# Optimization experiments

Measured on AMD Instinct MI355X. Metric: run time of the kernel, lower is better.

Reference implementation:

```python
import jax, jax.numpy as jnp
import numpy as np

HEADS = 4


def setup_inputs() -> dict:
    key = jax.random.key(0)
    ks = jax.random.split(key, 5)
    B, T, C, H, W = 2, 16, 256, 64, 64
    x = jax.random.normal(ks[0], (B, T, C, H, W), dtype=jnp.float32)
    s = 1.0 / np.sqrt(C).astype(np.float32)  # kaiming-ish init scale for 1x1 conv
    Wq = jax.random.normal(ks[1], (C, C), dtype=jnp.float32) * s
    Wk = jax.random.normal(ks[2], (C, C), dtype=jnp.float32) * s
    Wv = jax.random.normal(ks[3], (C, C), dtype=jnp.float32) * s
    Wp = jax.random.normal(ks[4], (C, C), dtype=jnp.float32) * s
    return {"x": x, "Wq": Wq, "Wk": Wk, "Wv": Wv, "Wp": Wp}


def reference(x, Wq, Wk, Wv, Wp):
    B, T, C, H, W = x.shape
    heads = HEADS
    Ch = C // heads
    scale = Ch ** (-0.5)
    # [B,T,C,H,W] -> [B*H*W, T, C]: each spatial pixel has a T x C temporal track
    xf = jnp.transpose(x, (0, 3, 4, 1, 2)).reshape(B * H * W, T, C)
    # Conv1d(C,C,1,bias=False) == channel matmul: out[n,t,d] = sum_c W[d,c] x[n,t,c]
    q = jnp.einsum('ntc,dc->ntd', xf, Wq).reshape(-1, T, heads, Ch) * scale
    k = jnp.einsum('ntc,dc->ntd', xf, Wk).reshape(-1, T, heads, Ch)
    v = jnp.einsum('ntc,dc->ntd', xf, Wv).reshape(-1, T, heads, Ch)
    k_soft = jax.nn.softmax(k, axis=1)    # softmax over time T (torch dim=-1 of [n,h,c,t])
    q_soft = jax.nn.softmax(q, axis=-1)   # softmax over head channels Ch (torch dim=-2)
    # linear attention: outer-product context then query contraction
    kv = jnp.einsum('nthc,nthd->nhcd', k_soft, v)         # [N,h,Ch,Ch]
    out = jnp.einsum('nthc,nhcd->nthd', q_soft, kv)       # [N,T,h,Ch]
    out = out.reshape(-1, T, C)
    out = jnp.einsum('ntc,dc->ntd', out, Wp)
    out = out.reshape(B, H, W, T, C)
    return jnp.transpose(out, (0, 3, 4, 1, 2))
```

## Files before the change

### kernel.cpp

```cpp
#include <hip/hip_runtime.h>
#include <hip/hip_bf16.h>

#define DI __device__ __forceinline__

typedef __attribute__((ext_vector_type(8))) short bf16x8;
typedef __attribute__((ext_vector_type(4))) float f32x4;
typedef __attribute__((ext_vector_type(4))) _Float16 f16x4;

constexpr int XPAD = 264;
constexpr float LOG2E = 1.4426950408889634f;

DI short f2bf(float f) {
  __hip_bfloat16 h = __float2bfloat16(f);
  union { __hip_bfloat16 h; short s; } c; c.h = h; return c.s;
}

DI unsigned pk2(float a, float b) {
  union { __hip_bfloat162 h; unsigned u; } c;
  c.h.x = __float2bfloat16(a); c.h.y = __float2bfloat16(b);
  return c.u;
}

DI short f2h(float f) {
  _Float16 h = (_Float16)f;
  union { _Float16 h; short s; } c; c.h = h; return c.s;
}

DI f16x4 pkh4(float a, float b, float c, float d) {
  auto lo = __builtin_amdgcn_cvt_pkrtz(a, b);
  auto hi = __builtin_amdgcn_cvt_pkrtz(c, d);
  union { struct { decltype(lo) l, h; } p; f16x4 v; } u;
  u.p.l = lo; u.p.h = hi;
  return u.v;
}

DI f16x4 ld4h(const short* p) {
  union { uint2 u; f16x4 v; } c;
  c.u = *(const uint2*)p;
  return c.v;
}

DI f32x4 mfma16(bf16x8 a, bf16x8 b, f32x4 c) {
  return __builtin_amdgcn_mfma_f32_16x16x32_bf16(a, b, c, 0, 0, 0);
}

DI f32x4 mfmah(f16x4 a, f16x4 b, f32x4 c) {
  return __builtin_amdgcn_mfma_f32_16x16x16f16(a, b, c, 0, 0, 0);
}

DI f32x4 fzero() { return f32x4{0.f, 0.f, 0.f, 0.f}; }

DI int xsw(int row, int e) { return row * 256 + (e ^ ((row & 7) << 3)); }

__global__ void wconv_kernel(const float* __restrict__ a, const float* __restrict__ b,
                             const float* __restrict__ c, const float* __restrict__ d,
                             short* __restrict__ o) {
  int i = blockIdx.x * 256 + threadIdx.x;
  int mat = i >> 14;
  int off = (i & 16383) * 4;
  const float* s = (mat == 0) ? a : (mat == 1) ? b : (mat == 2) ? c : d;
  const float sc = (mat == 0) ? 0.125f : 1.0f;
  float4 v = *(const float4*)(s + off);
  uint2 r; r.x = pk2(v.x * sc, v.y * sc); r.y = pk2(v.z * sc, v.w * sc);
  *(uint2*)(o + mat * 65536 + off) = r;
}

__global__ __launch_bounds__(256, 2)
void xt_kernel(const float* __restrict__ x, short* __restrict__ xt, int n0chunk) {
  __shared__ short T[64 * 258];
  const int tid = threadIdx.x;
  const int gi  = blockIdx.x >> 4;
  const int t   = blockIdx.x & 15;
  const int n0g = n0chunk + gi * 64;
  const int b   = n0g >> 12;
  const int hw0 = n0g & 4095;
  const float* xb = x + ((size_t)(b * 16 + t) * 256) * 4096 + hw0;

  #pragma unroll
  for (int ci = 0; ci < 16; ++ci) {
    const int c   = ci * 16 + (tid >> 4);
    const int px4 = tid & 15;
    float4 v = *(const float4*)(xb + (size_t)c * 4096 + px4 * 4);
    T[(px4 * 4 + 0) * 258 + c] = f2bf(v.x);
    T[(px4 * 4 + 1) * 258 + c] = f2bf(v.y);
    T[(px4 * 4 + 2) * 258 + c] = f2bf(v.z);
    T[(px4 * 4 + 3) * 258 + c] = f2bf(v.w);
  }
  __syncthreads();

  const int wave = tid >> 6, lane = tid & 63;
  #pragma unroll
  for (int itp = 0; itp < 16; ++itp) {
    const int px  = itp * 4 + wave;
    const int row = (px & 3) * 16 + t;
    const int sw8 = (row & 7) << 3;
    const size_t obase = ((size_t)(gi * 16 + (px >> 2))) * 16384 + row * 256;
    const int dstc = (((lane >> 1) * 8) ^ sw8) + (lane & 1) * 4;
    const int tb = px * 258 + lane * 4;
    union { short s[4]; uint2 u; } pk;
    pk.s[0] = T[tb + 0]; pk.s[1] = T[tb + 1];
    pk.s[2] = T[tb + 2]; pk.s[3] = T[tb + 3];
    *(uint2*)&xt[obase + dstc] = pk.u;
  }
}

__global__ __launch_bounds__(256, 3)
void k1_kernel(const short* __restrict__ xt, const short* __restrict__ wbf,
               short* __restrict__ att) {
  __shared__ short SMEM[16384 + 4096];
  short* Xs = SMEM;

  const int tid  = threadIdx.x;
  const int wave = tid >> 6;
  const int lane = tid & 63;
  const int g    = lane >> 4;
  const int li   = lane & 15;

  short* qs = SMEM + 16384 + wave * 1024;

  int bid = blockIdx.x;
  const int nb = gridDim.x;
  if ((nb & 7) == 0) { const int q = nb >> 3; bid = (bid & 7) * q + (bid >> 3); }

  {
    const short* src = xt + (size_t)bid * 16384 + wave * 512 + lane * 8;
    #pragma unroll
    for (int it = 0; it < 8; ++it) {
      __builtin_amdgcn_global_load_lds(
          (const __attribute__((address_space(1))) void*)(src + it * 2048),
          (__attribute__((address_space(3))) void*)(SMEM + it * 2048 + wave * 512),
          16, 0, 0);
    }
  }
  __syncthreads();

  const short* wq = wbf;
  const short* wk = wbf + 65536;
  const short* wv = wbf + 131072;
  const size_t wrow = (size_t)(wave * 64) * 256;

  f16x4 akf[4][4];
  {
    f32x4 kacc[4][4];
    #pragma unroll
    for (int p = 0; p < 4; ++p)
      #pragma unroll
      for (int nt = 0; nt < 4; ++nt) kacc[p][nt] = fzero();

    __builtin_amdgcn_s_setprio(1);
    #pragma unroll
    for (int ks = 0; ks < 8; ++ks) {
      bf16x8 kb[4];
      #pragma unroll
      for (int nt = 0; nt < 4; ++nt)
        kb[nt] = *(const bf16x8*)(wk + wrow + (size_t)(nt * 16 + li) * 256 + ks * 32 + g * 8);
      #pragma unroll
      for (int p = 0; p < 4; ++p) {
        bf16x8 af = *(const bf16x8*)&Xs[xsw(p * 16 + li, ks * 32 + g * 8)];
        #pragma unroll
        for (int nt = 0; nt < 4; ++nt)
          kacc[p][nt] = mfma16(af, kb[nt], kacc[p][nt]);
      }
    }
    __builtin_amdgcn_s_setprio(0);

    #pragma unroll
    for (int p = 0; p < 4; ++p)
      #pragma unroll
      for (int nt = 0; nt < 4; ++nt) {
        float e0 = exp2f(kacc[p][nt][0] * LOG2E);
        float e1 = exp2f(kacc[p][nt][1] * LOG2E);
        float e2 = exp2f(kacc[p][nt][2] * LOG2E);
        float e3 = exp2f(kacc[p][nt][3] * LOG2E);
        float s = e0 + e1 + e2 + e3;
        s += __shfl_xor(s, 16);
        s += __shfl_xor(s, 32);
        const float inv = 1.f / s;
        akf[p][nt] = pkh4(e0 * inv, e1 * inv, e2 * inv, e3 * inv);
      }
  }

  f16x4 bvf[4][4];
  #pragma unroll
  for (int h = 0; h < 2; ++h) {
    f32x4 vacc[4][2];
    #pragma unroll
    for (int p = 0; p < 4; ++p)
      #pragma unroll
      for (int n2 = 0; n2 < 2; ++n2) vacc[p][n2] = fzero();

    __builtin_amdgcn_s_setprio(1);
    #pragma unroll
    for (int ks = 0; ks < 8; ++ks) {
      bf16x8 vb[2];
      #pragma unroll
      for (int n2 = 0; n2 < 2; ++n2)
        vb[n2] = *(const bf16x8*)(wv + wrow + (size_t)((h * 2 + n2) * 16 + li) * 256 + ks * 32 + g * 8);
      #pragma unroll
      for (int p = 0; p < 4; ++p) {
        bf16x8 af = *(const bf16x8*)&Xs[xsw(p * 16 + li, ks * 32 + g * 8)];
        #pragma unroll
        for (int n2 = 0; n2 < 2; ++n2)
          vacc[p][n2] = mfma16(af, vb[n2], vacc[p][n2]);
      }
    }
    __builtin_amdgcn_s_setprio(0);

    #pragma unroll
    for (int p = 0; p < 4; ++p)
      #pragma unroll
      for (int n2 = 0; n2 < 2; ++n2)
        bvf[p][h * 2 + n2] = pkh4(vacc[p][n2][0], vacc[p][n2][1],
                                  vacc[p][n2][2], vacc[p][n2][3]);
  }

  f32x4 qacc[4][4];
  #pragma unroll
  for (int p = 0; p < 4; ++p)
    #pragma unroll
    for (int nt = 0; nt < 4; ++nt) qacc[p][nt] = fzero();

  __builtin_amdgcn_s_setprio(1);
  #pragma unroll
  for (int ks = 0; ks < 8; ++ks) {
    bf16x8 qb[4];
    #pragma unroll
    for (int nt = 0; nt < 4; ++nt)
      qb[nt] = *(const bf16x8*)(wq + wrow + (size_t)(nt * 16 + li) * 256 + ks * 32 + g * 8);
    #pragma unroll
    for (int p = 0; p < 4; ++p) {
      bf16x8 af = *(const bf16x8*)&Xs[xsw(p * 16 + li, ks * 32 + g * 8)];
      #pragma unroll
      for (int nt = 0; nt < 4; ++nt)
        qacc[p][nt] = mfma16(af, qb[nt], qacc[p][nt]);
    }
  }
  __builtin_amdgcn_s_setprio(0);

  #pragma unroll
  for (int p = 0; p < 4; ++p) {
    #pragma unroll
    for (int r = 0; r < 4; ++r) {
      float e0 = exp2f(qacc[p][0][r] * LOG2E);
      float e1 = exp2f(qacc[p][1][r] * LOG2E);
      float e2 = exp2f(qacc[p][2][r] * LOG2E);
      float e3 = exp2f(qacc[p][3][r] * LOG2E);
      float s = e0 + e1 + e2 + e3;
      s += __shfl_xor(s, 1); s += __shfl_xor(s, 2);
      s += __shfl_xor(s, 4); s += __shfl_xor(s, 8);
      const float inv = 1.f / s;
      const int t = g * 4 + r;
      const int xw = (t & 7) << 3;
      short* dq = qs + t * 64;
      dq[( 0 + li) ^ xw] = f2h(e0 * inv);
      dq[(16 + li) ^ xw] = f2h(e1 * inv);
      dq[(32 + li) ^ xw] = f2h(e2 * inv);
      dq[(48 + li) ^ xw] = f2h(e3 * inv);
    }

    f32x4 oacc[4];
    #pragma unroll
    for (int nt = 0; nt < 4; ++nt) oacc[nt] = fzero();

    #pragma unroll
    for (int cq = 0; cq < 4; ++cq) {
      f32x4 kva[4];
      #pragma unroll
      for (int nt = 0; nt < 4; ++nt)
        kva[nt] = mfmah(akf[p][cq], bvf[p][nt], fzero());
      f16x4 aq = ld4h(qs + li * 64 + (((cq * 16 + g * 4) ^ ((li & 7) << 3))));
      #pragma unroll
      for (int nt = 0; nt < 4; ++nt) {
        f16x4 kb16 = pkh4(kva[nt][0], kva[nt][1], kva[nt][2], kva[nt][3]);
        oacc[nt] = mfmah(aq, kb16, oacc[nt]);
      }
    }

    const size_t arow = ((size_t)bid * 4 + p) * 16;
    #pragma unroll
    for (int nt = 0; nt < 4; ++nt)
      #pragma unroll
      for (int r = 0; r < 4; ++r)
        att[(arow + g * 4 + r) * 256 + wave * 64 + nt * 16 + li] = f2bf(oacc[nt][r]);
  }
}

__global__ __launch_bounds__(256, 2)
void k2_kernel(const short* __restrict__ att, const short* __restrict__ wpb,
               float* __restrict__ out, int n0chunk) {
  __shared__ short A[128 * XPAD];
  const int tid = threadIdx.x;
  const int wave = tid >> 6, lane = tid & 63, g = lane >> 4, li = lane & 15;
  const int pb = blockIdx.x >> 1;
  const int t0 = (blockIdx.x & 1) * 8;
  const int n0 = n0chunk + pb * 16;
  const int b = n0 >> 12, hw0 = n0 & 4095;

  for (int idx = tid; idx < 128 * 32; idx += 256) {
    const int row = idx >> 5, seg = idx & 31;
    const int p = row & 15, tl = row >> 4;
    const short* src = att + ((size_t)((pb * 16 + p) * 16 + t0 + tl)) * 256 + seg * 8;
    *(int4*)&A[row * XPAD + seg * 8] = *(const int4*)src;
  }
  __syncthreads();

  f32x4 acc[8][4];
  #pragma unroll
  for (int mt = 0; mt < 8; ++mt)
    #pragma unroll
    for (int n4 = 0; n4 < 4; ++n4) acc[mt][n4] = fzero();

  #pragma unroll
  for (int ks = 0; ks < 8; ++ks) {
    bf16x8 bf[4];
    #pragma unroll
    for (int n4 = 0; n4 < 4; ++n4)
      bf[n4] = *(const bf16x8*)(wpb + (size_t)((wave * 4 + n4) * 16 + li) * 256 + ks * 32 + g * 8);
    #pragma unroll
    for (int mt = 0; mt < 8; ++mt) {
      bf16x8 af = *(const bf16x8*)&A[(mt * 16 + li) * XPAD + ks * 32 + g * 8];
      #pragma unroll
      for (int n4 = 0; n4 < 4; ++n4) acc[mt][n4] = mfma16(af, bf[n4], acc[mt][n4]);
    }
  }

  float* ob = out + (size_t)b * (16 * 256 * 4096) + hw0;
  #pragma unroll
  for (int mt = 0; mt < 8; ++mt)
    #pragma unroll
    for (int n4 = 0; n4 < 4; ++n4) {
      const int t = t0 + mt;
      const int c = (wave * 4 + n4) * 16 + li;
      float4 v;
      v.x = acc[mt][n4][0]; v.y = acc[mt][n4][1];
      v.z = acc[mt][n4][2]; v.w = acc[mt][n4][3];
      *(float4*)(ob + (size_t)(t * 256 + c) * 4096 + g * 4) = v;
    }
}

extern "C" void kernel_launch(void* const* d_in, const int* in_sizes, int n_in,
                              void* d_out, int out_size, void* d_ws, size_t ws_size,
                              hipStream_t stream) {
  const float* x  = (const float*)d_in[0];
  const float* Wq = (const float*)d_in[1];
  const float* Wk = (const float*)d_in[2];
  const float* Wv = (const float*)d_in[3];
  const float* Wp = (const float*)d_in[4];
  float* out = (float*)d_out;

  short* wbf = (short*)d_ws;
  short* att = wbf + 4 * 65536;

  wconv_kernel<<<256, 256, 0, stream>>>(Wq, Wk, Wv, Wp, wbf);

  const size_t wsAvail = (ws_size > 524288) ? (ws_size - 524288) : 0;
  const size_t perPix = 16 * 256 * 2;
  int chunk = 64;
  while (chunk < 8192 && (size_t)(chunk * 2) * perPix <= wsAvail) chunk <<= 1;

  short* xt = att + (size_t)chunk * 4096;

  for (int n0 = 0; n0 < 8192; n0 += chunk) {
    xt_kernel<<<(chunk / 64) * 16, 256, 0, stream>>>(x, xt, n0);
    k1_kernel<<<chunk / 4, 256, 0, stream>>>(xt, wbf, att);
    k2_kernel<<<(chunk / 16) * 2, 256, 0, stream>>>(att, wbf + 3 * 65536, out, n0);
  }
}
```

Before: 245.9 us.

## Compute q softmax first into global scratch, drop LDS q buffer for occupancy

Moves the Q projection and its channel softmax to the start of k1. The softmaxed q is written to a per-wave global scratch buffer instead of an LDS staging area, and k1 reads it back after a vmcnt wait. This frees LDS and register pressure so launch bounds can rise to 4 blocks per CU. It also replaces exp2f and division with the hardware exp2 and rcp intrinsics. In exchange it adds a global write and read round trip per pixel. It also needs more workspace, which may shrink the chunk size and add kernel launches. Cross-lane visibility through global memory is relied on within a wave.

```diff
diff --git a/kernel.cpp b/kernel.cpp
--- a/kernel.cpp
+++ b/kernel.cpp
@@ -9,6 +9,9 @@
 
 constexpr int XPAD = 264;
 constexpr float LOG2E = 1.4426950408889634f;
+
+DI float fexp(float x) { return __builtin_amdgcn_exp2f(x * LOG2E); }
+DI float frcp(float x) { return __builtin_amdgcn_rcpf(x); }
 
 DI short f2bf(float f) {
   __hip_bfloat16 h = __float2bfloat16(f);
@@ -104,10 +107,10 @@
   }
 }
 
-__global__ __launch_bounds__(256, 3)
+__global__ __launch_bounds__(256, 4)
 void k1_kernel(const short* __restrict__ xt, const short* __restrict__ wbf,
-               short* __restrict__ att) {
-  __shared__ short SMEM[16384 + 4096];
+               short* __restrict__ att, short* __restrict__ qsg) {
+  __shared__ short SMEM[16384];
   short* Xs = SMEM;
 
   const int tid  = threadIdx.x;
@@ -116,8 +119,6 @@
   const int g    = lane >> 4;
   const int li   = lane & 15;
 
-  short* qs = SMEM + 16384 + wave * 1024;
-
   int bid = blockIdx.x;
   const int nb = gridDim.x;
   if ((nb & 7) == 0) { const int q = nb >> 3; bid = (bid & 7) * q + (bid >> 3); }
@@ -138,6 +139,54 @@
   const short* wk = wbf + 65536;
   const short* wv = wbf + 131072;
   const size_t wrow = (size_t)(wave * 64) * 256;
+  short* qsw = qsg + ((size_t)bid * 4 * 4 + wave) * 1024;
+
+  {
+    f32x4 qacc[4][4];
+    #pragma unroll
+    for (int p = 0; p < 4; ++p)
+      #pragma unroll
+      for (int nt = 0; nt < 4; ++nt) qacc[p][nt] = fzero();
+
+    __builtin_amdgcn_s_setprio(1);
+    #pragma unroll
+    for (int ks = 0; ks < 8; ++ks) {
+      bf16x8 qb[4];
+      #pragma unroll
+      for (int nt = 0; nt < 4; ++nt)
+        qb[nt] = *(const bf16x8*)(wq + wrow + (size_t)(nt * 16 + li) * 256 + ks * 32 + g * 8);
+      #pragma unroll
+      for (int p = 0; p < 4; ++p) {
+        bf16x8 af = *(const bf16x8*)&Xs[xsw(p * 16 + li, ks * 32 + g * 8)];
+        #pragma unroll
+        for (int nt = 0; nt < 4; ++nt)
+          qacc[p][nt] = mfma16(af, qb[nt], qacc[p][nt]);
+      }
+    }
+    __builtin_amdgcn_s_setprio(0);
+
+    #pragma unroll
+    for (int p = 0; p < 4; ++p) {
+      short* qsp = qsw + p * 4096;
+      #pragma unroll
+      for (int r = 0; r < 4; ++r) {
+        float e0 = fexp(qacc[p][0][r]);
+        float e1 = fexp(qacc[p][1][r]);
+        float e2 = fexp(qacc[p][2][r]);
+        float e3 = fexp(qacc[p][3][r]);
+        float s = e0 + e1 + e2 + e3;
+        s += __shfl_xor(s, 1); s += __shfl_xor(s, 2);
+        s += __shfl_xor(s, 4); s += __shfl_xor(s, 8);
+        const float inv = frcp(s);
+        const int t = g * 4 + r;
+        short* dst = qsp + t * 64 + li;
+        dst[0]  = f2h(e0 * inv);
+        dst[16] = f2h(e1 * inv);
+        dst[32] = f2h(e2 * inv);
+        dst[48] = f2h(e3 * inv);
+      }
+    }
+  }
 
   f16x4 akf[4][4];
   {
@@ -168,14 +217,14 @@
     for (int p = 0; p < 4; ++p)
       #pragma unroll
       for (int nt = 0; nt < 4; ++nt) {
-        float e0 = exp2f(kacc[p][nt][0] * LOG2E);
-        float e1 = exp2f(kacc[p][nt][1] * LOG2E);
-        float e2 = exp2f(kacc[p][nt][2] * LOG2E);
-        float e3 = exp2f(kacc[p][nt][3] * LOG2E);
+        float e0 = fexp(kacc[p][nt][0]);
+        float e1 = fexp(kacc[p][nt][1]);
+        float e2 = fexp(kacc[p][nt][2]);
+        float e3 = fexp(kacc[p][nt][3]);
         float s = e0 + e1 + e2 + e3;
         s += __shfl_xor(s, 16);
         s += __shfl_xor(s, 32);
-        const float inv = 1.f / s;
+        const float inv = frcp(s);
         akf[p][nt] = pkh4(e0 * inv, e1 * inv, e2 * inv, e3 * inv);
       }
   }
@@ -214,50 +263,11 @@
                                   vacc[p][n2][2], vacc[p][n2][3]);
   }
 
-  f32x4 qacc[4][4];
-  #pragma unroll
-  for (int p = 0; p < 4; ++p)
-    #pragma unroll
-    for (int nt = 0; nt < 4; ++nt) qacc[p][nt] = fzero();
-
-  __builtin_amdgcn_s_setprio(1);
-  #pragma unroll
-  for (int ks = 0; ks < 8; ++ks) {
-    bf16x8 qb[4];
-    #pragma unroll
-    for (int nt = 0; nt < 4; ++nt)
-      qb[nt] = *(const bf16x8*)(wq + wrow + (size_t)(nt * 16 + li) * 256 + ks * 32 + g * 8);
-    #pragma unroll
-    for (int p = 0; p < 4; ++p) {
-      bf16x8 af = *(const bf16x8*)&Xs[xsw(p * 16 + li, ks * 32 + g * 8)];
-      #pragma unroll
-      for (int nt = 0; nt < 4; ++nt)
-        qacc[p][nt] = mfma16(af, qb[nt], qacc[p][nt]);
-    }
-  }
-  __builtin_amdgcn_s_setprio(0);
+  asm volatile("s_waitcnt vmcnt(0)" ::: "memory");
 
   #pragma unroll
   for (int p = 0; p < 4; ++p) {
-    #pragma unroll
-    for (int r = 0; r < 4; ++r) {
-      float e0 = exp2f(qacc[p][0][r] * LOG2E);
-      float e1 = exp2f(qacc[p][1][r] * LOG2E);
-      float e2 = exp2f(qacc[p][2][r] * LOG2E);
-      float e3 = exp2f(qacc[p][3][r] * LOG2E);
-      float s = e0 + e1 + e2 + e3;
-      s += __shfl_xor(s, 1); s += __shfl_xor(s, 2);
-      s += __shfl_xor(s, 4); s += __shfl_xor(s, 8);
-      const float inv = 1.f / s;
-      const int t = g * 4 + r;
-      const int xw = (t & 7) << 3;
-      short* dq = qs + t * 64;
-      dq[( 0 + li) ^ xw] = f2h(e0 * inv);
-      dq[(16 + li) ^ xw] = f2h(e1 * inv);
-      dq[(32 + li) ^ xw] = f2h(e2 * inv);
-      dq[(48 + li) ^ xw] = f2h(e3 * inv);
-    }
-
+    const short* qsp = qsw + p * 4096;
     f32x4 oacc[4];
     #pragma unroll
     for (int nt = 0; nt < 4; ++nt) oacc[nt] = fzero();
@@ -268,7 +278,7 @@
       #pragma unroll
       for (int nt = 0; nt < 4; ++nt)
         kva[nt] = mfmah(akf[p][cq], bvf[p][nt], fzero());
-      f16x4 aq = ld4h(qs + li * 64 + (((cq * 16 + g * 4) ^ ((li & 7) << 3))));
+      f16x4 aq = ld4h(qsp + li * 64 + cq * 16 + g * 4);
       #pragma unroll
       for (int nt = 0; nt < 4; ++nt) {
         f16x4 kb16 = pkh4(kva[nt][0], kva[nt][1], kva[nt][2], kva[nt][3]);
@@ -356,13 +366,14 @@
   const size_t wsAvail = (ws_size > 524288) ? (ws_size - 524288) : 0;
   const size_t perPix = 16 * 256 * 2;
   int chunk = 64;
-  while (chunk < 8192 && (size_t)(chunk * 2) * perPix <= wsAvail) chunk <<= 1;
-
-  short* xt = att + (size_t)chunk * 4096;
+  while (chunk < 8192 && (size_t)(chunk * 3) * perPix <= wsAvail) chunk <<= 1;
+
+  short* xtb = att + (size_t)chunk * 4096;
+  short* qsg = xtb + (size_t)chunk * 4096;
 
   for (int n0 = 0; n0 < 8192; n0 += chunk) {
-    xt_kernel<<<(chunk / 64) * 16, 256, 0, stream>>>(x, xt, n0);
-    k1_kernel<<<chunk / 4, 256, 0, stream>>>(xt, wbf, att);
+    xt_kernel<<<(chunk / 64) * 16, 256, 0, stream>>>(x, xtb, n0);
+    k1_kernel<<<chunk / 4, 256, 0, stream>>>(xtb, wbf, att, qsg);
     k2_kernel<<<(chunk / 16) * 2, 256, 0, stream>>>(att, wbf + 3 * 65536, out, n0);
   }
 }
```

Measured after the change: 252.7 us. 1.03x slower.
